# Kernel optimization log

Hardware: AMD Instinct MI355X
Metric: run time of the kernel (lower is better)

The kernel has to match this reference:

```python
import jax, jax.numpy as jnp
import numpy as np

B, K, C = 64, 19, 384
HF, WF = 16, 16          # F_map spatial size (stride-32)
HS, WS = 256, 256        # seg_weights spatial size
REGION_DIM = 256


def setup_inputs() -> dict:
    key = jax.random.key(0)
    k1, k2, k3, k4 = jax.random.split(key, 4)
    F_map = jax.random.normal(k1, (B, C, HF, WF), dtype=jnp.float32)
    seg_weights = jax.random.uniform(k2, (B, K, HS, WS), dtype=jnp.float32)
    # torch.nn.Linear(384, region_dim): W [out, in], b [out]
    W = jax.random.normal(k3, (REGION_DIM, C), dtype=jnp.float32) * (1.0 / np.sqrt(C))
    b = jax.random.normal(k4, (REGION_DIM,), dtype=jnp.float32) * 0.01
    return {"F_map": F_map, "seg_weights": seg_weights, "W": W, "b": b}


def reference(F_map, seg_weights, W, b):
    Bsz, Ch, Hf, Wf = F_map.shape
    Kc = seg_weights.shape[1]
    # bilinear resize, half-pixel centers == torch align_corners=False, no antialias
    w = jax.image.resize(seg_weights, (Bsz, Kc, Hf, Wf), method="bilinear", antialias=False)
    # (F_map[:,None] * w[:,:,None]).mean((-2,-1))  ==  einsum / (Hf*Wf)
    region_feats = jnp.einsum("bchw,bkhw->bkc", F_map, w) / (Hf * Wf)  # [B,K,C]
    global_feat = jnp.mean(F_map, axis=(-2, -1))[:, None, :]            # [B,1,C]
    all_feats = jnp.concatenate([region_feats, global_feat], axis=1)    # [B,K+1,C]
    projected = jax.nn.relu(jnp.einsum("bkc,dc->bkd", all_feats, W) + b)
    return projected.reshape(Bsz, -1)  # [B, (K+1)*region_dim]
```

## Files before the change

### kernel.cpp

```cpp
#include <hip/hip_runtime.h>

#define BB   64
#define KSEG 19
#define CC   384
#define HS   256
#define DD   256
#define KP1  20

__global__ __launch_bounds__(256) void k_downsample(const float* __restrict__ seg,
                                                    float* __restrict__ wds) {
    int idx = blockIdx.x * 256 + threadIdx.x;
    int j  = idx & 15;
    int i  = (idx >> 4) & 15;
    int bk = idx >> 8;
    const float* S  = seg + (size_t)bk * (HS * HS);
    const float* p0 = S + (16 * i + 7) * HS + (16 * j + 7);
    const float* p1 = p0 + HS;
    wds[idx] = 0.25f * (p0[0] + p0[1] + p1[0] + p1[1]);
}

__global__ __launch_bounds__(256) void k_feats(const float* __restrict__ F,
                                               const float* __restrict__ wds,
                                               float* __restrict__ feats) {
    __shared__ float wS[KP1][256];
    __shared__ float Ft[128][65];
    const int t  = threadIdx.x;
    const int b  = blockIdx.y;
    const int c0 = blockIdx.x * 128;

    const float* wb = wds + (size_t)b * (KSEG * 256);
    for (int e = t; e < KP1 * 256; e += 256) {
        (&wS[0][0])[e] = (e < KSEG * 256) ? wb[e] : 1.0f;
    }

    const int c_lane = t & 63;
    const int kg     = t >> 6;
    const float* Fb  = F + ((size_t)b * CC + c0) * 256;
    float acc[5][2] = {};

    for (int pt = 0; pt < 4; ++pt) {
        __syncthreads();
        {
            int row  = t >> 1;
            int base = (t & 1) * 32;
            const float* src = Fb + row * 256 + pt * 64 + base;
#pragma unroll
            for (int q = 0; q < 8; ++q) {
                float4 v = *(const float4*)(src + q * 4);
                float* dst = &Ft[row][base + q * 4];
                dst[0] = v.x; dst[1] = v.y; dst[2] = v.z; dst[3] = v.w;
            }
        }
        __syncthreads();
        const int pb = pt * 64;
#pragma unroll 4
        for (int pp = 0; pp < 64; ++pp) {
            float f0 = Ft[c_lane][pp];
            float f1 = Ft[c_lane + 64][pp];
#pragma unroll
            for (int kk = 0; kk < 5; ++kk) {
                float wv = wS[kg * 5 + kk][pb + pp];
                acc[kk][0] += f0 * wv;
                acc[kk][1] += f1 * wv;
            }
        }
    }

    const float inv = 1.0f / 256.0f;
#pragma unroll
    for (int kk = 0; kk < 5; ++kk) {
        int k = kg * 5 + kk;
        float* o = feats + ((size_t)b * KP1 + k) * CC + c0 + c_lane;
        o[0]  = acc[kk][0] * inv;
        o[64] = acc[kk][1] * inv;
    }
}

__global__ __launch_bounds__(256) void k_project(const float* __restrict__ feats,
                                                 const float* __restrict__ W,
                                                 const float* __restrict__ bias,
                                                 float* __restrict__ out) {
    __shared__ float fS[KP1][CC];
    __shared__ float Wt[128][65];
    const int t  = threadIdx.x;
    const int b  = blockIdx.y;
    const int d0 = blockIdx.x * 128;

    const float* fb = feats + (size_t)b * KP1 * CC;
    for (int e = t; e < KP1 * CC; e += 256) {
        (&fS[0][0])[e] = fb[e];
    }

    const int d_lane = t & 63;
    const int kg     = t >> 6;
    float acc[5][2] = {};

    for (int ct = 0; ct < 6; ++ct) {
        __syncthreads();
        {
            int row  = t >> 1;
            int base = (t & 1) * 32;
            const float* src = W + (size_t)(d0 + row) * CC + ct * 64 + base;
#pragma unroll
            for (int q = 0; q < 8; ++q) {
                float4 v = *(const float4*)(src + q * 4);
                float* dst = &Wt[row][base + q * 4];
                dst[0] = v.x; dst[1] = v.y; dst[2] = v.z; dst[3] = v.w;
            }
        }
        __syncthreads();
        const int cb = ct * 64;
#pragma unroll 4
        for (int cc = 0; cc < 64; ++cc) {
            float w0 = Wt[d_lane][cc];
            float w1 = Wt[d_lane + 64][cc];
#pragma unroll
            for (int kk = 0; kk < 5; ++kk) {
                float fv = fS[kg * 5 + kk][cb + cc];
                acc[kk][0] += w0 * fv;
                acc[kk][1] += w1 * fv;
            }
        }
    }

    float b0 = bias[d0 + d_lane];
    float b1 = bias[d0 + 64 + d_lane];
#pragma unroll
    for (int kk = 0; kk < 5; ++kk) {
        int k = kg * 5 + kk;
        float* o = out + ((size_t)b * KP1 + k) * DD + d0 + d_lane;
        float v0 = acc[kk][0] + b0;
        float v1 = acc[kk][1] + b1;
        o[0]  = v0 > 0.0f ? v0 : 0.0f;
        o[64] = v1 > 0.0f ? v1 : 0.0f;
    }
}

extern "C" void kernel_launch(void* const* d_in, const int* in_sizes, int n_in,
                              void* d_out, int out_size, void* d_ws, size_t ws_size,
                              hipStream_t stream) {
    const float* F    = (const float*)d_in[0];
    const float* seg  = (const float*)d_in[1];
    const float* W    = (const float*)d_in[2];
    const float* bias = (const float*)d_in[3];
    float* out = (float*)d_out;

    float* wds   = (float*)d_ws;
    float* feats = wds + (size_t)BB * KSEG * 256;

    k_downsample<<<dim3((BB * KSEG * 256) / 256), dim3(256), 0, stream>>>(seg, wds);
    k_feats    <<<dim3(3, BB), dim3(256), 0, stream>>>(F, wds, feats);
    k_project  <<<dim3(2, BB), dim3(256), 0, stream>>>(feats, W, bias, out);
}
```

Before: 404.7 us.

## Coalesce downsample row loads and halve tile width in feats/project kernels

The downsample kernel now assigns one block per (batch, segment) map. It loads only the 32 needed source rows into shared memory with coalesced float4 reads, replacing scattered per-thread 2x2 loads. The feats and projection kernels now use 64-wide channel/output tiles, which doubles the grid. Their inner loops read float4 vectors from shared memory with one accumulator per k. This trades register reuse per thread for more blocks and wider LDS reads, though some LDS bank conflicts may come from the padded rows.

```diff
diff --git a/kernel.cpp b/kernel.cpp
--- a/kernel.cpp
+++ b/kernel.cpp
@@ -9,59 +9,67 @@
 
 __global__ __launch_bounds__(256) void k_downsample(const float* __restrict__ seg,
                                                     float* __restrict__ wds) {
-    int idx = blockIdx.x * 256 + threadIdx.x;
-    int j  = idx & 15;
-    int i  = (idx >> 4) & 15;
-    int bk = idx >> 8;
-    const float* S  = seg + (size_t)bk * (HS * HS);
-    const float* p0 = S + (16 * i + 7) * HS + (16 * j + 7);
-    const float* p1 = p0 + HS;
-    wds[idx] = 0.25f * (p0[0] + p0[1] + p1[0] + p1[1]);
+    __shared__ __align__(16) float rows[32][257];
+    const int t  = threadIdx.x;
+    const int bk = blockIdx.x;
+    const float* S = seg + (size_t)bk * (HS * HS);
+
+#pragma unroll
+    for (int it = 0; it < 8; ++it) {
+        int f   = it * 256 + t;
+        int r   = f >> 6;
+        int c4  = f & 63;
+        int grow = 16 * (r >> 1) + 7 + (r & 1);
+        float4 v = *(const float4*)(S + grow * HS + c4 * 4);
+        float* dst = &rows[r][c4 * 4];
+        dst[0] = v.x; dst[1] = v.y; dst[2] = v.z; dst[3] = v.w;
+    }
+    __syncthreads();
+
+    int j = t & 15, i = t >> 4;
+    float s = rows[2*i    ][16*j + 7] + rows[2*i    ][16*j + 8]
+            + rows[2*i + 1][16*j + 7] + rows[2*i + 1][16*j + 8];
+    wds[bk * 256 + t] = 0.25f * s;
 }
 
 __global__ __launch_bounds__(256) void k_feats(const float* __restrict__ F,
                                                const float* __restrict__ wds,
                                                float* __restrict__ feats) {
-    __shared__ float wS[KP1][256];
-    __shared__ float Ft[128][65];
+    __shared__ __align__(16) float wS[KP1][256];
+    __shared__ __align__(16) float Ft[64][65];
     const int t  = threadIdx.x;
     const int b  = blockIdx.y;
-    const int c0 = blockIdx.x * 128;
+    const int c0 = blockIdx.x * 64;
 
     const float* wb = wds + (size_t)b * (KSEG * 256);
-    for (int e = t; e < KP1 * 256; e += 256) {
+    for (int e = t; e < KP1 * 256; e += 256)
         (&wS[0][0])[e] = (e < KSEG * 256) ? wb[e] : 1.0f;
-    }
 
     const int c_lane = t & 63;
     const int kg     = t >> 6;
     const float* Fb  = F + ((size_t)b * CC + c0) * 256;
-    float acc[5][2] = {};
+    float acc[5] = {};
 
     for (int pt = 0; pt < 4; ++pt) {
         __syncthreads();
-        {
-            int row  = t >> 1;
-            int base = (t & 1) * 32;
-            const float* src = Fb + row * 256 + pt * 64 + base;
 #pragma unroll
-            for (int q = 0; q < 8; ++q) {
-                float4 v = *(const float4*)(src + q * 4);
-                float* dst = &Ft[row][base + q * 4];
-                dst[0] = v.x; dst[1] = v.y; dst[2] = v.z; dst[3] = v.w;
-            }
+        for (int it = 0; it < 4; ++it) {
+            int f  = it * 256 + t;
+            int r  = f >> 4;
+            int c4 = f & 15;
+            float4 v = *(const float4*)(Fb + r * 256 + pt * 64 + c4 * 4);
+            float* dst = &Ft[r][c4 * 4];
+            dst[0] = v.x; dst[1] = v.y; dst[2] = v.z; dst[3] = v.w;
         }
         __syncthreads();
-        const int pb = pt * 64;
 #pragma unroll 4
-        for (int pp = 0; pp < 64; ++pp) {
-            float f0 = Ft[c_lane][pp];
-            float f1 = Ft[c_lane + 64][pp];
+        for (int q4 = 0; q4 < 16; ++q4) {
+            const float* fp = &Ft[c_lane][q4 * 4];
+            float f0 = fp[0], f1 = fp[1], f2 = fp[2], f3 = fp[3];
 #pragma unroll
             for (int kk = 0; kk < 5; ++kk) {
-                float wv = wS[kg * 5 + kk][pb + pp];
-                acc[kk][0] += f0 * wv;
-                acc[kk][1] += f1 * wv;
+                float4 wv = *(const float4*)&wS[kg * 5 + kk][pt * 64 + q4 * 4];
+                acc[kk] += f0 * wv.x + f1 * wv.y + f2 * wv.z + f3 * wv.w;
             }
         }
     }
@@ -70,9 +78,7 @@
 #pragma unroll
     for (int kk = 0; kk < 5; ++kk) {
         int k = kg * 5 + kk;
-        float* o = feats + ((size_t)b * KP1 + k) * CC + c0 + c_lane;
-        o[0]  = acc[kk][0] * inv;
-        o[64] = acc[kk][1] * inv;
+        feats[((size_t)b * KP1 + k) * CC + c0 + c_lane] = acc[kk] * inv;
     }
 }
 
@@ -80,59 +86,57 @@
                                                  const float* __restrict__ W,
                                                  const float* __restrict__ bias,
                                                  float* __restrict__ out) {
-    __shared__ float fS[KP1][CC];
-    __shared__ float Wt[128][65];
+    __shared__ __align__(16) float fS[KP1][CC];
+    __shared__ __align__(16) float Wt[64][65];
     const int t  = threadIdx.x;
     const int b  = blockIdx.y;
-    const int d0 = blockIdx.x * 128;
+    const int d0 = blockIdx.x * 64;
 
     const float* fb = feats + (size_t)b * KP1 * CC;
-    for (int e = t; e < KP1 * CC; e += 256) {
-        (&fS[0][0])[e] = fb[e];
+#pragma unroll
+    for (int it = 0; it < 8; ++it) {
+        int f = it * 256 + t;
+        if (f < (KP1 * CC) / 4) {
+            float4 v = *(const float4*)(fb + f * 4);
+            float* dst = &(&fS[0][0])[f * 4];
+            dst[0] = v.x; dst[1] = v.y; dst[2] = v.z; dst[3] = v.w;
+        }
     }
 
     const int d_lane = t & 63;
     const int kg     = t >> 6;
-    float acc[5][2] = {};
+    float acc[5] = {};
 
     for (int ct = 0; ct < 6; ++ct) {
         __syncthreads();
-        {
-            int row  = t >> 1;
-            int base = (t & 1) * 32;
-            const float* src = W + (size_t)(d0 + row) * CC + ct * 64 + base;
 #pragma unroll
-            for (int q = 0; q < 8; ++q) {
-                float4 v = *(const float4*)(src + q * 4);
-                float* dst = &Wt[row][base + q * 4];
-                dst[0] = v.x; dst[1] = v.y; dst[2] = v.z; dst[3] = v.w;
-            }
+        for (int it = 0; it < 4; ++it) {
+            int f  = it * 256 + t;
+            int r  = f >> 4;
+            int c4 = f & 15;
+            float4 v = *(const float4*)(W + (size_t)(d0 + r) * CC + ct * 64 + c4 * 4);
+            float* dst = &Wt[r][c4 * 4];
+            dst[0] = v.x; dst[1] = v.y; dst[2] = v.z; dst[3] = v.w;
         }
         __syncthreads();
-        const int cb = ct * 64;
 #pragma unroll 4
-        for (int cc = 0; cc < 64; ++cc) {
-            float w0 = Wt[d_lane][cc];
-            float w1 = Wt[d_lane + 64][cc];
+        for (int q4 = 0; q4 < 16; ++q4) {
+            const float* wp = &Wt[d_lane][q4 * 4];
+            float w0 = wp[0], w1 = wp[1], w2 = wp[2], w3 = wp[3];
 #pragma unroll
             for (int kk = 0; kk < 5; ++kk) {
-                float fv = fS[kg * 5 + kk][cb + cc];
-                acc[kk][0] += w0 * fv;
-                acc[kk][1] += w1 * fv;
+                float4 fv = *(const float4*)&fS[kg * 5 + kk][ct * 64 + q4 * 4];
+                acc[kk] += w0 * fv.x + w1 * fv.y + w2 * fv.z + w3 * fv.w;
             }
         }
     }
 
-    float b0 = bias[d0 + d_lane];
-    float b1 = bias[d0 + 64 + d_lane];
+    float bv = bias[d0 + d_lane];
 #pragma unroll
     for (int kk = 0; kk < 5; ++kk) {
         int k = kg * 5 + kk;
-        float* o = out + ((size_t)b * KP1 + k) * DD + d0 + d_lane;
-        float v0 = acc[kk][0] + b0;
-        float v1 = acc[kk][1] + b1;
-        o[0]  = v0 > 0.0f ? v0 : 0.0f;
-        o[64] = v1 > 0.0f ? v1 : 0.0f;
+        float v = acc[kk] + bv;
+        out[((size_t)b * KP1 + k) * DD + d0 + d_lane] = v > 0.0f ? v : 0.0f;
     }
 }
 
@@ -148,7 +152,7 @@
     float* wds   = (float*)d_ws;
     float* feats = wds + (size_t)BB * KSEG * 256;
 
-    k_downsample<<<dim3((BB * KSEG * 256) / 256), dim3(256), 0, stream>>>(seg, wds);
-    k_feats    <<<dim3(3, BB), dim3(256), 0, stream>>>(F, wds, feats);
-    k_project  <<<dim3(2, BB), dim3(256), 0, stream>>>(feats, W, bias, out);
+    k_downsample<<<dim3(BB * KSEG), dim3(256), 0, stream>>>(seg, wds);
+    k_feats    <<<dim3(6, BB), dim3(256), 0, stream>>>(F, wds, feats);
+    k_project  <<<dim3(4, BB), dim3(256), 0, stream>>>(feats, W, bias, out);
 }
```

Result: faster. 391.5 us (-3.3%).
